# Kernel tuning notes

Hardware: AMD Instinct MI355X
Metric: run time of the kernel (lower is better)

The kernel has to match this reference:

```python
import jax, jax.numpy as jnp
import numpy as np

# conv_ada hyperparameters from init_kwargs: ka=1, alpha=0.25, kw=0.2
KA1 = 1.0          # activation scale for conv1 (ka)
KA2 = 1.25         # activation scale for conv2 (ka + alpha)
KW = 0.2           # weight clipping threshold used by the binary weight STE


def ste_sign(x, clip=1.0):
    """Binary sign with straight-through estimator (hardtanh-style clip).
    Forward value is sign(x); gradient is that of clip(x, -clip, clip)."""
    xc = jnp.clip(x, -clip, clip)
    return xc + jax.lax.stop_gradient(jnp.sign(x) - xc)


def conv_bin(x, w, ka, kw):
    """1-bit activation / 1-bit weight 3x3 conv (conv_ada).
    Activations -> ka * sign(x); weights -> per-out-channel mean(|w|) * sign(w)."""
    xq = ka * ste_sign(x)
    alpha_w = jnp.mean(jnp.abs(w), axis=(1, 2, 3), keepdims=True)  # [O,1,1,1]
    wq = alpha_w * ste_sign(w, kw)
    return jax.lax.conv_general_dilated(
        xq, wq, window_strides=(1, 1), padding='SAME',
        dimension_numbers=('NCHW', 'OIHW', 'NCHW'))


def prelu(x, slope):
    # per-channel PReLU, slope shape [C]
    return jnp.where(x >= 0, x, slope[None, :, None, None] * x)


def pixel_shuffle(x, r=2):
    b, c, h, w = x.shape
    co = c // (r * r)
    x = x.reshape(b, co, r, r, h, w)
    x = x.transpose(0, 1, 4, 2, 5, 3)  # b, co, h, r, w, r
    return x.reshape(b, co, h * r, w * r)


def setup_inputs() -> dict:
    key = jax.random.key(0)
    ks = jax.random.split(key, 11)
    B, C, H, W = 8, 64, 256, 256
    return {
        'x': jax.random.normal(ks[0], (B, C, H, W), jnp.float32),
        'w1': jax.random.normal(ks[1], (C, C, 3, 3), jnp.float32) * 0.1,
        'w2': jax.random.normal(ks[2], (2 * C, C, 3, 3), jnp.float32) * 0.1,
        'b_in': jax.random.normal(ks[3], (1, C, 1, 1), jnp.float32) * 0.01,
        'b1': jax.random.normal(ks[4], (1, C, 1, 1), jnp.float32) * 0.01,
        's1': jax.random.uniform(ks[5], (C,), jnp.float32) * 0.25,
        'b2': jax.random.normal(ks[6], (1, C, 1, 1), jnp.float32) * 0.01,
        'b2_': jax.random.normal(ks[7], (1, C, 1, 1), jnp.float32) * 0.01,
        'b3': jax.random.normal(ks[8], (1, 2 * C, 1, 1), jnp.float32) * 0.01,
        's2': jax.random.uniform(ks[9], (2 * C,), jnp.float32) * 0.25,
        'b4': jax.random.normal(ks[10], (1, 2 * C, 1, 1), jnp.float32) * 0.01,
    }


def reference(x, w1, w2, b_in, b1, s1, b2, b2_, b3, s2, b4):
    out = conv_bin(x + b_in, w1, KA1, KW)       # move1_ -> conv1
    xres = out + x                              # residual x = out + x
    # NOTE: in the original forward, move1 -> prelu1 -> move2 are computed on
    # `out` and then immediately overwritten by out = move2_(x); that branch
    # is dead code and does not affect the output (b1, s1, b2 get zero grads).
    out = conv_bin(xres + b2_, w2, KA2, KW)     # move2_ -> conv2
    out = out + jnp.concatenate([xres, xres], axis=1)  # shortcut = cat(x, x)
    out = prelu(out + b3, s2) + b4              # move3 -> prelu2 -> move4
    return pixel_shuffle(out, 2)                # [B, C/2, 2H, 2W]
```

## Files before the change

kernel.cpp:

```cpp
#include <hip/hip_runtime.h>
#include <hip/hip_bf16.h>

typedef unsigned long long u64;
typedef unsigned int u32;
typedef unsigned short ushort8 __attribute__((ext_vector_type(8)));
typedef unsigned short ushortx16 __attribute__((ext_vector_type(16)));
typedef u64 u64x2 __attribute__((ext_vector_type(2)));
typedef u64 u64x4 __attribute__((ext_vector_type(4)));
typedef float fx2 __attribute__((ext_vector_type(2)));
typedef float fx4 __attribute__((ext_vector_type(4)));

#define IMG_H 256
#define IMG_W 256
#define CIN   64
#define HW    (IMG_H * IMG_W)
#define NPIX  (8 * HW)

static __device__ __forceinline__ float bf16bits_to_f32(unsigned short h) {
    union { u32 u; float f; } c;
    c.u = ((u32)h) << 16;
    return c.f;
}
static __device__ __forceinline__ unsigned short f32_to_bf16bits(float f) {
    __hip_bfloat16 hb = __float2bfloat16(f);
    return *(unsigned short*)&hb;
}

__global__ void prep_kernel(const float* __restrict__ w1,
                            const float* __restrict__ w2,
                            u64* __restrict__ w1b, float* __restrict__ a1,
                            u64* __restrict__ w2b, float* __restrict__ a2) {
    int blk = blockIdx.x;
    int lane = threadIdx.x;
    const float* w;
    u64* wb;
    float* al;
    if (blk < 64) { w = w1 + (size_t)blk * 576;        wb = w1b + blk * 9;        al = a1 + blk; }
    else          { w = w2 + (size_t)(blk - 64) * 576; wb = w2b + (blk - 64) * 9; al = a2 + (blk - 64); }

    const float* wi = w + lane * 9;
    float s = 0.f;
    u64 bits[9];
#pragma unroll
    for (int t = 0; t < 9; ++t) {
        float v = wi[t];
        s += fabsf(v);
        bits[t] = __ballot(v > 0.f);
    }
#pragma unroll
    for (int m = 32; m >= 1; m >>= 1) s += __shfl_xor(s, m);
    if (lane == 0) {
        *al = s * (1.f / 576.f);
#pragma unroll
        for (int t = 0; t < 9; ++t) wb[t] = bits[t];
    }
}

__global__ __launch_bounds__(256)
void pack_kernel(const float* __restrict__ x,
                 const float* __restrict__ b_in,
                 u64* __restrict__ bits1) {
    int tid = blockIdx.x * 256 + threadIdx.x;
    int n = tid >> 14;
    int p = (tid & 16383) * 4;
    const float* xp = x + (size_t)n * CIN * HW + p;
    u32 lo[4] = {0, 0, 0, 0}, hi[4] = {0, 0, 0, 0};
#pragma unroll
    for (int c = 0; c < 32; ++c) {
        fx4 v = *(const fx4*)(xp + (size_t)c * HW);
        float b = b_in[c];
#pragma unroll
        for (int q = 0; q < 4; ++q) lo[q] |= (u32)((v[q] + b) > 0.f) << c;
    }
#pragma unroll
    for (int c = 0; c < 32; ++c) {
        fx4 v = *(const fx4*)(xp + (size_t)(c + 32) * HW);
        float b = b_in[c + 32];
#pragma unroll
        for (int q = 0; q < 4; ++q) hi[q] |= (u32)((v[q] + b) > 0.f) << c;
    }
    u64x4 pk;
#pragma unroll
    for (int q = 0; q < 4; ++q) pk[q] = ((u64)hi[q] << 32) | lo[q];
    *(u64x4*)(bits1 + (size_t)n * HW + p) = pk;
}

__global__ __launch_bounds__(256)
void conv1_kernel(const float* __restrict__ x,
                  const float* __restrict__ b2_,
                  const u64* __restrict__ bits1,
                  const u64* __restrict__ wbits,
                  const float* __restrict__ alpha1,
                  ushort8* __restrict__ xres,
                  u64* __restrict__ bits2) {
    int i = blockIdx.x * 256 + threadIdx.x;
    int n = i >> 16, p = i & 65535;
    int y = p >> 8, xc = p & 255;

    u64 xb[9];
    int invmask = 0, nv = 0;
#pragma unroll
    for (int t = 0; t < 9; ++t) {
        int dy = t / 3 - 1, dx = t % 3 - 1;
        bool v = ((unsigned)(y + dy) < (unsigned)IMG_H) &
                 ((unsigned)(xc + dx) < (unsigned)IMG_W);
        xb[t] = v ? bits1[i + dy * IMG_W + dx] : 0ull;
        invmask |= (v ? 0 : 1) << t;
        nv += v ? 1 : 0;
    }

    const float* xp = x + (size_t)n * CIN * HW + p;

    float rv[64];
#pragma unroll
    for (int c = 0; c < 64; ++c)
        rv[c] = xp[(size_t)c * HW];
    __builtin_amdgcn_sched_barrier(0);

    u64 w2 = 0;
#pragma unroll
    for (int g = 0; g < 8; ++g) {
        ushort8 pk;
        u32 gm = 0;
#pragma unroll
        for (int j = 0; j < 8; ++j) {
            int o = g * 8 + j;
            const u64* wo = wbits + o * 9;
            int D = 0;
#pragma unroll
            for (int t = 0; t < 9; ++t) D += __popcll(xb[t] ^ wo[t]);
            int S = 64 * nv - 2 * D;
            if (invmask) {
#pragma unroll
                for (int t = 0; t < 9; ++t)
                    if ((invmask >> t) & 1) S += 2 * __popcll(wo[t]);
            }
            float r = alpha1[o] * (float)S + rv[o];
            pk[j] = f32_to_bf16bits(r);
            gm |= (u32)((r + b2_[o]) > 0.f) << j;
        }
        xres[(size_t)(n * 8 + g) * HW + p] = pk;
        w2 |= (u64)gm << (8 * g);
    }
    bits2[i] = w2;
}

__global__ __launch_bounds__(256)
void conv2_kernel(const ushort8* __restrict__ xres,
                  const u64* __restrict__ bits2,
                  const u64* __restrict__ wbits,
                  const float* __restrict__ alpha2,
                  const float* __restrict__ b3,
                  const float* __restrict__ s2,
                  const float* __restrict__ b4,
                  float* __restrict__ out) {
    int tid = blockIdx.x * 256 + threadIdx.x;
    int n = tid >> 15;
    int p = (tid & 32767) * 2;
    int y = p >> 8, xc = p & 255;

    u64 W[3][4];
    const u64* bp = bits2 + (size_t)n * HW;
#pragma unroll
    for (int r = 0; r < 3; ++r) {
        int yy = y - 1 + r;
        bool rv = (unsigned)yy < (unsigned)IMG_H;
        const u64* row = bp + yy * IMG_W + xc;
        W[r][0] = (rv && xc > 0)   ? row[-1] : 0ull;
        W[r][1] = rv ? row[0] : 0ull;
        W[r][2] = rv ? row[1] : 0ull;
        W[r][3] = (rv && xc < 254) ? row[2]  : 0ull;
    }
    int inv0 = 0, inv1 = 0, nv0 = 0, nv1 = 0;
#pragma unroll
    for (int t = 0; t < 9; ++t) {
        const int r = t / 3, c = t % 3;
        bool rv = (unsigned)(y - 1 + r) < (unsigned)IMG_H;
        bool v0 = rv && !(c == 0 && xc == 0);
        bool v1 = rv && !(c == 2 && xc == 254);
        inv0 |= (v0 ? 0 : 1) << t; nv0 += v0 ? 1 : 0;
        inv1 |= (v1 ? 0 : 1) << t; nv1 += v1 ? 1 : 0;
    }
    const int edge = inv0 | inv1;

    const ushortx16* xrp = (const ushortx16*)(xres + (size_t)n * 8 * HW + p);
    float* ob = out + (size_t)n * 32 * 512 * 512;
    const int Y = 2 * y, X = 2 * xc;

    ushortx16 xr0 = xrp[0 * (HW / 2)];
    ushortx16 xr1 = xrp[1 * (HW / 2)];
    ushortx16 xr2 = xrp[2 * (HW / 2)];
    ushortx16 xr3 = xrp[3 * (HW / 2)];
    ushortx16 xr4 = xrp[4 * (HW / 2)];
    ushortx16 xr5 = xrp[5 * (HW / 2)];
    ushortx16 xr6 = xrp[6 * (HW / 2)];
    ushortx16 xr7 = xrp[7 * (HW / 2)];
    __builtin_amdgcn_sched_barrier(0);

    auto comp = [&](const ushortx16& xr, int g) {
#pragma unroll
        for (int jj = 0; jj < 8; jj += 2) {
            float lo4[4], hi4[4];
#pragma unroll
            for (int q = 0; q < 2; ++q) {
                int o = g * 8 + jj + q;
                float xrv0 = bf16bits_to_f32(xr[jj + q]);
                float xrv1 = bf16bits_to_f32(xr[8 + jj + q]);
                {
                    const u64* wo = wbits + o * 9;
                    int D0 = 0, D1 = 0;
#pragma unroll
                    for (int t = 0; t < 9; ++t) {
                        const int r = t / 3, c = t % 3;
                        u64 w = wo[t];
                        D0 += __popcll(W[r][c] ^ w);
                        D1 += __popcll(W[r][c + 1] ^ w);
                    }
                    int S0 = 64 * nv0 - 2 * D0;
                    int S1 = 64 * nv1 - 2 * D1;
                    if (edge) {
#pragma unroll
                        for (int t = 0; t < 9; ++t) {
                            int pw = __popcll(wo[t]);
                            if ((inv0 >> t) & 1) S0 += 2 * pw;
                            if ((inv1 >> t) & 1) S1 += 2 * pw;
                        }
                    }
                    float ka = 1.25f * alpha2[o], bb = b3[o], ss = s2[o], b4v = b4[o];
                    float u0 = ka * (float)S0 + xrv0 + bb;
                    float u1 = ka * (float)S1 + xrv1 + bb;
                    u0 = (u0 >= 0.f) ? u0 : ss * u0;
                    u1 = (u1 >= 0.f) ? u1 : ss * u1;
                    lo4[q] = u0 + b4v;
                    lo4[2 + q] = u1 + b4v;
                }
                {
                    int o2 = o + 64;
                    const u64* wo = wbits + o2 * 9;
                    int D0 = 0, D1 = 0;
#pragma unroll
                    for (int t = 0; t < 9; ++t) {
                        const int r = t / 3, c = t % 3;
                        u64 w = wo[t];
                        D0 += __popcll(W[r][c] ^ w);
                        D1 += __popcll(W[r][c + 1] ^ w);
                    }
                    int S0 = 64 * nv0 - 2 * D0;
                    int S1 = 64 * nv1 - 2 * D1;
                    if (edge) {
#pragma unroll
                        for (int t = 0; t < 9; ++t) {
                            int pw = __popcll(wo[t]);
                            if ((inv0 >> t) & 1) S0 += 2 * pw;
                            if ((inv1 >> t) & 1) S1 += 2 * pw;
                        }
                    }
                    float ka = 1.25f * alpha2[o2], bb = b3[o2], ss = s2[o2], b4v = b4[o2];
                    float u0 = ka * (float)S0 + xrv0 + bb;
                    float u1 = ka * (float)S1 + xrv1 + bb;
                    u0 = (u0 >= 0.f) ? u0 : ss * u0;
                    u1 = (u1 >= 0.f) ? u1 : ss * u1;
                    hi4[q] = u0 + b4v;
                    hi4[2 + q] = u1 + b4v;
                }
            }
            int o = g * 8 + jj;
            int co = o >> 2;
            int r1 = (o >> 1) & 1;
            fx4 vl; vl.x = lo4[0]; vl.y = lo4[1]; vl.z = lo4[2]; vl.w = lo4[3];
            fx4 vh; vh.x = hi4[0]; vh.y = hi4[1]; vh.z = hi4[2]; vh.w = hi4[3];
            __builtin_nontemporal_store(
                vl, (fx4*)(ob + ((size_t)co * 512 + Y + r1) * 512 + X));
            __builtin_nontemporal_store(
                vh, (fx4*)(ob + ((size_t)(co + 16) * 512 + Y + r1) * 512 + X));
        }
    };

    comp(xr0, 0); comp(xr1, 1); comp(xr2, 2); comp(xr3, 3);
    comp(xr4, 4); comp(xr5, 5); comp(xr6, 6); comp(xr7, 7);
}

extern "C" void kernel_launch(void* const* d_in, const int* in_sizes, int n_in,
                              void* d_out, int out_size, void* d_ws, size_t ws_size,
                              hipStream_t stream) {
    const float* x    = (const float*)d_in[0];
    const float* w1   = (const float*)d_in[1];
    const float* w2   = (const float*)d_in[2];
    const float* b_in = (const float*)d_in[3];
    const float* b2_  = (const float*)d_in[7];
    const float* b3   = (const float*)d_in[8];
    const float* s2   = (const float*)d_in[9];
    const float* b4   = (const float*)d_in[10];
    float* out = (float*)d_out;

    char* ws = (char*)d_ws;
    u64*   w1b   = (u64*)(ws + 0);
    u64*   w2b   = (u64*)(ws + 4608);
    float* a1    = (float*)(ws + 13824);
    float* a2    = (float*)(ws + 14080);
    u64*   bits1 = (u64*)(ws + 16384);
    u64*   bits2 = (u64*)(ws + 16384 + 4194304);
    ushort8* xres = (ushort8*)(ws + 16384 + 2 * 4194304);

    prep_kernel<<<192, 64, 0, stream>>>(w1, w2, w1b, a1, w2b, a2);

    pack_kernel <<<NPIX / 1024, 256, 0, stream>>>(x, b_in, bits1);
    conv1_kernel<<<NPIX / 256, 256, 0, stream>>>(x, b2_, bits1, w1b, a1, xres, bits2);
    conv2_kernel<<<NPIX / 512, 256, 0, stream>>>(xres, bits2, w2b, a2, b3, s2, b4, out);
}
```

Measured before the change: 224.9 us.

## Fuse pack, conv1 and conv2 into one tiled kernel with LDS halos

Replaces the three per-pixel kernels with one kernel over 32x16 spatial tiles. Each tile packs sign bits of x with a 2-pixel halo into LDS, computes conv1 bits for the interior plus a recomputed 1-pixel halo ring, and runs conv2 directly from LDS. This removes the global round trips of bits1, bits2 and the bf16 xres intermediate. In exchange it adds halo recomputation, block-level syncs and strided scalar loads of x during packing.

```diff
diff --git a/kernel.cpp b/kernel.cpp
--- a/kernel.cpp
+++ b/kernel.cpp
@@ -3,10 +3,7 @@
 
 typedef unsigned long long u64;
 typedef unsigned int u32;
-typedef unsigned short ushort8 __attribute__((ext_vector_type(8)));
 typedef unsigned short ushortx16 __attribute__((ext_vector_type(16)));
-typedef u64 u64x2 __attribute__((ext_vector_type(2)));
-typedef u64 u64x4 __attribute__((ext_vector_type(4)));
 typedef float fx2 __attribute__((ext_vector_type(2)));
 typedef float fx4 __attribute__((ext_vector_type(4)));
 
@@ -14,7 +11,7 @@
 #define IMG_W 256
 #define CIN   64
 #define HW    (IMG_H * IMG_W)
-#define NPIX  (8 * HW)
+
 
 static __device__ __forceinline__ float bf16bits_to_f32(unsigned short h) {
     union { u32 u; float f; } c;
@@ -56,146 +53,179 @@
     }
 }
 
-__global__ __launch_bounds__(256)
-void pack_kernel(const float* __restrict__ x,
-                 const float* __restrict__ b_in,
-                 u64* __restrict__ bits1) {
-    int tid = blockIdx.x * 256 + threadIdx.x;
-    int n = tid >> 14;
-    int p = (tid & 16383) * 4;
-    const float* xp = x + (size_t)n * CIN * HW + p;
-    u32 lo[4] = {0, 0, 0, 0}, hi[4] = {0, 0, 0, 0};
-#pragma unroll
-    for (int c = 0; c < 32; ++c) {
-        fx4 v = *(const fx4*)(xp + (size_t)c * HW);
-        float b = b_in[c];
-#pragma unroll
-        for (int q = 0; q < 4; ++q) lo[q] |= (u32)((v[q] + b) > 0.f) << c;
-    }
-#pragma unroll
-    for (int c = 0; c < 32; ++c) {
-        fx4 v = *(const fx4*)(xp + (size_t)(c + 32) * HW);
-        float b = b_in[c + 32];
-#pragma unroll
-        for (int q = 0; q < 4; ++q) hi[q] |= (u32)((v[q] + b) > 0.f) << c;
-    }
-    u64x4 pk;
-#pragma unroll
-    for (int q = 0; q < 4; ++q) pk[q] = ((u64)hi[q] << 32) | lo[q];
-    *(u64x4*)(bits1 + (size_t)n * HW + p) = pk;
-}
-
-__global__ __launch_bounds__(256)
-void conv1_kernel(const float* __restrict__ x,
+__global__ __launch_bounds__(256, 3)
+void fused_kernel(const float* __restrict__ x,
+                  const float* __restrict__ b_in,
                   const float* __restrict__ b2_,
-                  const u64* __restrict__ bits1,
-                  const u64* __restrict__ wbits,
+                  const u64* __restrict__ w1bits,
                   const float* __restrict__ alpha1,
-                  ushort8* __restrict__ xres,
-                  u64* __restrict__ bits2) {
-    int i = blockIdx.x * 256 + threadIdx.x;
-    int n = i >> 16, p = i & 65535;
-    int y = p >> 8, xc = p & 255;
-
-    u64 xb[9];
-    int invmask = 0, nv = 0;
-#pragma unroll
-    for (int t = 0; t < 9; ++t) {
-        int dy = t / 3 - 1, dx = t % 3 - 1;
-        bool v = ((unsigned)(y + dy) < (unsigned)IMG_H) &
-                 ((unsigned)(xc + dx) < (unsigned)IMG_W);
-        xb[t] = v ? bits1[i + dy * IMG_W + dx] : 0ull;
-        invmask |= (v ? 0 : 1) << t;
-        nv += v ? 1 : 0;
-    }
-
-    const float* xp = x + (size_t)n * CIN * HW + p;
-
-    float rv[64];
-#pragma unroll
-    for (int c = 0; c < 64; ++c)
-        rv[c] = xp[(size_t)c * HW];
-    __builtin_amdgcn_sched_barrier(0);
-
-    u64 w2 = 0;
-#pragma unroll
-    for (int g = 0; g < 8; ++g) {
-        ushort8 pk;
-        u32 gm = 0;
-#pragma unroll
-        for (int j = 0; j < 8; ++j) {
-            int o = g * 8 + j;
-            const u64* wo = wbits + o * 9;
-            int D = 0;
-#pragma unroll
-            for (int t = 0; t < 9; ++t) D += __popcll(xb[t] ^ wo[t]);
-            int S = 64 * nv - 2 * D;
-            if (invmask) {
-#pragma unroll
-                for (int t = 0; t < 9; ++t)
-                    if ((invmask >> t) & 1) S += 2 * __popcll(wo[t]);
-            }
-            float r = alpha1[o] * (float)S + rv[o];
-            pk[j] = f32_to_bf16bits(r);
-            gm |= (u32)((r + b2_[o]) > 0.f) << j;
-        }
-        xres[(size_t)(n * 8 + g) * HW + p] = pk;
-        w2 |= (u64)gm << (8 * g);
-    }
-    bits2[i] = w2;
-}
-
-__global__ __launch_bounds__(256)
-void conv2_kernel(const ushort8* __restrict__ xres,
-                  const u64* __restrict__ bits2,
-                  const u64* __restrict__ wbits,
+                  const u64* __restrict__ w2bits,
                   const float* __restrict__ alpha2,
                   const float* __restrict__ b3,
                   const float* __restrict__ s2,
                   const float* __restrict__ b4,
                   float* __restrict__ out) {
-    int tid = blockIdx.x * 256 + threadIdx.x;
-    int n = tid >> 15;
-    int p = (tid & 32767) * 2;
-    int y = p >> 8, xc = p & 255;
-
-    u64 W[3][4];
-    const u64* bp = bits2 + (size_t)n * HW;
-#pragma unroll
-    for (int r = 0; r < 3; ++r) {
-        int yy = y - 1 + r;
-        bool rv = (unsigned)yy < (unsigned)IMG_H;
-        const u64* row = bp + yy * IMG_W + xc;
-        W[r][0] = (rv && xc > 0)   ? row[-1] : 0ull;
-        W[r][1] = rv ? row[0] : 0ull;
-        W[r][2] = rv ? row[1] : 0ull;
-        W[r][3] = (rv && xc < 254) ? row[2]  : 0ull;
-    }
+    __shared__ u64 b1lds[20][36];
+    __shared__ u64 b2lds[18][34];
+
+    const int tid = threadIdx.x;
+    const int n = blockIdx.z;
+    const int tx0 = blockIdx.x * 32;
+    const int ty0 = blockIdx.y * 16;
+    const float* xn = x + (size_t)n * CIN * HW;
+
+    for (int idx = tid; idx < 720; idx += 256) {
+        int ly = idx / 36, lx = idx - ly * 36;
+        int gy = ty0 + ly - 2, gx = tx0 + lx - 2;
+        u64 w = 0;
+        if ((unsigned)gy < (unsigned)IMG_H && (unsigned)gx < (unsigned)IMG_W) {
+            const float* p = xn + gy * IMG_W + gx;
+            u32 lo = 0, hi = 0;
+#pragma unroll
+            for (int c = 0; c < 32; ++c)
+                lo |= (u32)((p[(size_t)c * HW] + b_in[c]) > 0.f) << c;
+#pragma unroll
+            for (int c = 0; c < 32; ++c)
+                hi |= (u32)((p[(size_t)(c + 32) * HW] + b_in[c + 32]) > 0.f) << c;
+            w = ((u64)hi << 32) | lo;
+        }
+        b1lds[ly][lx] = w;
+    }
+    __syncthreads();
+
+    if (tid < 100) {
+        int ly, lx;
+        if (tid < 34)      { ly = 0;  lx = tid; }
+        else if (tid < 68) { ly = 17; lx = tid - 34; }
+        else { int r2 = tid - 68; ly = 1 + (r2 >> 1); lx = (r2 & 1) ? 33 : 0; }
+        int gy = ty0 + ly - 1, gx = tx0 + lx - 1;
+        u64 w2w = 0;
+        if ((unsigned)gy < (unsigned)IMG_H && (unsigned)gx < (unsigned)IMG_W) {
+            u64 xb[9];
+            int invmask = 0, nv = 0;
+#pragma unroll
+            for (int t = 0; t < 9; ++t) {
+                int dy = t / 3 - 1, dx = t % 3 - 1;
+                bool v = ((unsigned)(gy + dy) < (unsigned)IMG_H) &
+                         ((unsigned)(gx + dx) < (unsigned)IMG_W);
+                xb[t] = b1lds[ly + 1 + dy][lx + 1 + dx];
+                invmask |= (v ? 0 : 1) << t;
+                nv += v ? 1 : 0;
+            }
+            const float* xp = xn + gy * IMG_W + gx;
+#pragma unroll
+            for (int g = 0; g < 8; ++g) {
+                u32 gm = 0;
+#pragma unroll
+                for (int j = 0; j < 8; ++j) {
+                    int o = g * 8 + j;
+                    const u64* wo = w1bits + o * 9;
+                    int D = 0;
+#pragma unroll
+                    for (int t = 0; t < 9; ++t) D += __popcll(xb[t] ^ wo[t]);
+                    int S = 64 * nv - 2 * D;
+                    if (invmask) {
+#pragma unroll
+                        for (int t = 0; t < 9; ++t)
+                            if ((invmask >> t) & 1) S += 2 * __popcll(wo[t]);
+                    }
+                    float r = alpha1[o] * (float)S + xp[(size_t)o * HW];
+                    gm |= (u32)((r + b2_[o]) > 0.f) << j;
+                }
+                w2w |= (u64)gm << (8 * g);
+            }
+        }
+        b2lds[ly][lx] = w2w;
+    }
+
+    const int py = tid >> 4, k = tid & 15;
+    const int gy = ty0 + py;
+    const int gx0 = tx0 + 2 * k;
+
+    u64 W1[3][4];
+#pragma unroll
+    for (int r = 0; r < 3; ++r)
+#pragma unroll
+        for (int c = 0; c < 4; ++c)
+            W1[r][c] = b1lds[py + 1 + r][2 * k + 1 + c];
+
     int inv0 = 0, inv1 = 0, nv0 = 0, nv1 = 0;
 #pragma unroll
     for (int t = 0; t < 9; ++t) {
-        const int r = t / 3, c = t % 3;
-        bool rv = (unsigned)(y - 1 + r) < (unsigned)IMG_H;
-        bool v0 = rv && !(c == 0 && xc == 0);
-        bool v1 = rv && !(c == 2 && xc == 254);
+        int r = t / 3, c = t % 3;
+        bool rv = (unsigned)(gy - 1 + r) < (unsigned)IMG_H;
+        bool v0 = rv && ((unsigned)(gx0 - 1 + c) < (unsigned)IMG_W);
+        bool v1 = rv && ((unsigned)(gx0 + c) < (unsigned)IMG_W);
         inv0 |= (v0 ? 0 : 1) << t; nv0 += v0 ? 1 : 0;
         inv1 |= (v1 ? 0 : 1) << t; nv1 += v1 ? 1 : 0;
     }
     const int edge = inv0 | inv1;
 
-    const ushortx16* xrp = (const ushortx16*)(xres + (size_t)n * 8 * HW + p);
+    const float* xp = xn + gy * IMG_W + gx0;
+    u64 wc0 = 0, wc1 = 0;
+
+    auto c1g = [&](int g, u64& w0acc, u64& w1acc) -> ushortx16 {
+        ushortx16 pk;
+        u32 g0 = 0, g1 = 0;
+#pragma unroll
+        for (int j = 0; j < 8; ++j) {
+            int o = g * 8 + j;
+            const u64* wo = w1bits + o * 9;
+            int D0 = 0, D1 = 0;
+#pragma unroll
+            for (int t = 0; t < 9; ++t) {
+                int r = t / 3, c = t % 3;
+                u64 w = wo[t];
+                D0 += __popcll(W1[r][c] ^ w);
+                D1 += __popcll(W1[r][c + 1] ^ w);
+            }
+            int S0 = 64 * nv0 - 2 * D0;
+            int S1 = 64 * nv1 - 2 * D1;
+            if (edge) {
+#pragma unroll
+                for (int t = 0; t < 9; ++t) {
+                    int pw = __popcll(wo[t]);
+                    if ((inv0 >> t) & 1) S0 += 2 * pw;
+                    if ((inv1 >> t) & 1) S1 += 2 * pw;
+                }
+            }
+            fx2 v = *(const fx2*)(xp + (size_t)o * HW);
+            float a = alpha1[o];
+            float r0 = a * (float)S0 + v.x;
+            float r1 = a * (float)S1 + v.y;
+            pk[j]     = f32_to_bf16bits(r0);
+            pk[8 + j] = f32_to_bf16bits(r1);
+            float bv = b2_[o];
+            g0 |= (u32)((r0 + bv) > 0.f) << j;
+            g1 |= (u32)((r1 + bv) > 0.f) << j;
+        }
+        w0acc |= (u64)g0 << (8 * g);
+        w1acc |= (u64)g1 << (8 * g);
+        return pk;
+    };
+
+    ushortx16 xr0 = c1g(0, wc0, wc1);
+    ushortx16 xr1 = c1g(1, wc0, wc1);
+    ushortx16 xr2 = c1g(2, wc0, wc1);
+    ushortx16 xr3 = c1g(3, wc0, wc1);
+    ushortx16 xr4 = c1g(4, wc0, wc1);
+    ushortx16 xr5 = c1g(5, wc0, wc1);
+    ushortx16 xr6 = c1g(6, wc0, wc1);
+    ushortx16 xr7 = c1g(7, wc0, wc1);
+
+    b2lds[py + 1][2 * k + 1] = wc0;
+    b2lds[py + 1][2 * k + 2] = wc1;
+    __syncthreads();
+
+    u64 W2[3][4];
+#pragma unroll
+    for (int r = 0; r < 3; ++r)
+#pragma unroll
+        for (int c = 0; c < 4; ++c)
+            W2[r][c] = b2lds[py + r][2 * k + c];
+
     float* ob = out + (size_t)n * 32 * 512 * 512;
-    const int Y = 2 * y, X = 2 * xc;
-
-    ushortx16 xr0 = xrp[0 * (HW / 2)];
-    ushortx16 xr1 = xrp[1 * (HW / 2)];
-    ushortx16 xr2 = xrp[2 * (HW / 2)];
-    ushortx16 xr3 = xrp[3 * (HW / 2)];
-    ushortx16 xr4 = xrp[4 * (HW / 2)];
-    ushortx16 xr5 = xrp[5 * (HW / 2)];
-    ushortx16 xr6 = xrp[6 * (HW / 2)];
-    ushortx16 xr7 = xrp[7 * (HW / 2)];
-    __builtin_amdgcn_sched_barrier(0);
+    const int Y = 2 * gy, X = 2 * gx0;
 
     auto comp = [&](const ushortx16& xr, int g) {
 #pragma unroll
@@ -207,14 +237,14 @@
                 float xrv0 = bf16bits_to_f32(xr[jj + q]);
                 float xrv1 = bf16bits_to_f32(xr[8 + jj + q]);
                 {
-                    const u64* wo = wbits + o * 9;
+                    const u64* wo = w2bits + o * 9;
                     int D0 = 0, D1 = 0;
 #pragma unroll
                     for (int t = 0; t < 9; ++t) {
-                        const int r = t / 3, c = t % 3;
+                        int r = t / 3, c = t % 3;
                         u64 w = wo[t];
-                        D0 += __popcll(W[r][c] ^ w);
-                        D1 += __popcll(W[r][c + 1] ^ w);
+                        D0 += __popcll(W2[r][c] ^ w);
+                        D1 += __popcll(W2[r][c + 1] ^ w);
                     }
                     int S0 = 64 * nv0 - 2 * D0;
                     int S1 = 64 * nv1 - 2 * D1;
@@ -236,14 +266,14 @@
                 }
                 {
                     int o2 = o + 64;
-                    const u64* wo = wbits + o2 * 9;
+                    const u64* wo = w2bits + o2 * 9;
                     int D0 = 0, D1 = 0;
 #pragma unroll
                     for (int t = 0; t < 9; ++t) {
-                        const int r = t / 3, c = t % 3;
+                        int r = t / 3, c = t % 3;
                         u64 w = wo[t];
-                        D0 += __popcll(W[r][c] ^ w);
-                        D1 += __popcll(W[r][c + 1] ^ w);
+                        D0 += __popcll(W2[r][c] ^ w);
+                        D1 += __popcll(W2[r][c + 1] ^ w);
                     }
                     int S0 = 64 * nv0 - 2 * D0;
                     int S1 = 64 * nv1 - 2 * D1;
@@ -294,17 +324,14 @@
     float* out = (float*)d_out;
 
     char* ws = (char*)d_ws;
-    u64*   w1b   = (u64*)(ws + 0);
-    u64*   w2b   = (u64*)(ws + 4608);
-    float* a1    = (float*)(ws + 13824);
-    float* a2    = (float*)(ws + 14080);
-    u64*   bits1 = (u64*)(ws + 16384);
-    u64*   bits2 = (u64*)(ws + 16384 + 4194304);
-    ushort8* xres = (ushort8*)(ws + 16384 + 2 * 4194304);
+    u64*   w1b = (u64*)(ws + 0);
+    u64*   w2b = (u64*)(ws + 4608);
+    float* a1  = (float*)(ws + 13824);
+    float* a2  = (float*)(ws + 14080);
 
     prep_kernel<<<192, 64, 0, stream>>>(w1, w2, w1b, a1, w2b, a2);
 
-    pack_kernel <<<NPIX / 1024, 256, 0, stream>>>(x, b_in, bits1);
-    conv1_kernel<<<NPIX / 256, 256, 0, stream>>>(x, b2_, bits1, w1b, a1, xres, bits2);
-    conv2_kernel<<<NPIX / 512, 256, 0, stream>>>(xres, bits2, w2b, a2, b3, s2, b4, out);
-}
+    dim3 grid(IMG_W / 32, IMG_H / 16, 8);
+    fused_kernel<<<grid, 256, 0, stream>>>(x, b_in, b2_, w1b, a1, w2b, a2,
+                                           b3, s2, b4, out);
+}
```

Result: slower. 380.6 us (+69.2%).
